# Kernel tuning notes

Measured on AMD Instinct MI355X. Metric: run time of the kernel, lower is better.

Reference implementation:

```python
import jax, jax.numpy as jnp
import numpy as np

N_HEADS = 16
N_UNITS = 1024
B, S = 4, 1024


def setup_inputs() -> dict:
    key = jax.random.key(0)
    ks = jax.random.split(key, 12)
    std = 0.02
    query = jax.random.normal(ks[0], (B, S, N_UNITS), dtype=jnp.float32)
    key_t = jax.random.normal(ks[1], (B, S, N_UNITS), dtype=jnp.float32)
    value = jax.random.normal(ks[2], (B, S, N_UNITS), dtype=jnp.float32)
    # causal mask [B, S, S]; forward does mask.unsqueeze(1) -> broadcast over heads
    mask = jnp.broadcast_to(jnp.tril(jnp.ones((S, S), dtype=jnp.int32)), (B, S, S))
    Wq = jax.random.normal(ks[3], (N_UNITS, N_UNITS), dtype=jnp.float32) * std
    bq = jnp.zeros((N_UNITS,), dtype=jnp.float32)
    Wk = jax.random.normal(ks[4], (N_UNITS, N_UNITS), dtype=jnp.float32) * std
    bk = jnp.zeros((N_UNITS,), dtype=jnp.float32)
    Wv = jax.random.normal(ks[5], (N_UNITS, N_UNITS), dtype=jnp.float32) * std
    bv = jnp.zeros((N_UNITS,), dtype=jnp.float32)
    Wo = jax.random.normal(ks[6], (N_UNITS, N_UNITS), dtype=jnp.float32) * std
    bo = jnp.zeros((N_UNITS,), dtype=jnp.float32)
    return {"query": query, "key": key_t, "value": value, "mask": mask,
            "Wq": Wq, "bq": bq, "Wk": Wk, "bk": bk, "Wv": Wv, "bv": bv,
            "Wo": Wo, "bo": bo}


def reference(query, key, value, mask, Wq, bq, Wk, bk, Wv, bv, Wo, bo):
    b, s, u = query.shape
    h = N_HEADS
    dk = u // h
    # projections (torch Linear: x @ W.T + b), split into heads -> [b, h, s, dk]
    q = (query @ Wq.T + bq).reshape(b, s, h, dk).transpose(0, 2, 1, 3)
    k = (key @ Wk.T + bk).reshape(b, s, h, dk).transpose(0, 2, 1, 3)
    v = (value @ Wv.T + bv).reshape(b, s, h, dk).transpose(0, 2, 1, 3)
    # NOTE: original divides by sqrt(d_k) twice -> net scale 1/d_k (faithful)
    scores = jnp.einsum('bhqd,bhkd->bhqk', q, k) / jnp.float32(dk)
    scores = jnp.where(mask[:, None, :, :] == 0, jnp.float32(-1e9), scores)
    attn = jax.nn.softmax(scores, axis=-1)  # dropout = identity (eval mode)
    out = jnp.einsum('bhqk,bhkd->bhqd', attn, v)
    out = out.transpose(0, 2, 1, 3).reshape(b, s, u)
    return out @ Wo.T + bo
```

## Files before the change

### kernel.cpp

```cpp
#include <hip/hip_runtime.h>
#include <stdint.h>

#define NH 16
#define DK 64
#define NB 4
#define SS 1024
#define UU 1024

typedef __attribute__((ext_vector_type(8))) __bf16 bf16x8;
typedef __attribute__((ext_vector_type(4))) float f32x4;

__device__ inline short f2bf(float f) {
  union { float f; uint32_t u; } c; c.f = f;
  uint32_t u = c.u;
  uint32_t r = (u + 0x7fffu + ((u >> 16) & 1u)) >> 16;
  return (short)(uint16_t)r;
}

__global__ void cvt_multi(const float* __restrict__ s0, const float* __restrict__ s1,
                          const float* __restrict__ s2, const float* __restrict__ s3,
                          short* __restrict__ dst, int n4each) {
  const int z = blockIdx.z;
  const float* s = (z == 0) ? s0 : (z == 1) ? s1 : (z == 2) ? s2 : s3;
  int i = blockIdx.x * blockDim.x + threadIdx.x;
  if (i >= n4each) return;
  const float4 v = reinterpret_cast<const float4*>(s)[i];
  short4 o;
  o.x = f2bf(v.x); o.y = f2bf(v.y); o.z = f2bf(v.z); o.w = f2bf(v.w);
  reinterpret_cast<short4*>(dst + (size_t)z * n4each * 4)[i] = o;
}

template <int ROWS>
__device__ inline void stage_rows(short* lds, const short* gsrc, int ld) {
  const int t = threadIdx.x;
  const int w = t >> 6;
  constexpr int ROUNDS = ROWS / 64;
#pragma unroll
  for (int r = 0; r < ROUNDS; ++r) {
    int idx = r * 256 + t;
    const short* src = gsrc + (size_t)(idx >> 2) * ld + (idx & 3) * 8;
    __builtin_amdgcn_global_load_lds(
        (const __attribute__((address_space(1))) void*)src,
        (__attribute__((address_space(3))) void*)(lds + (size_t)(r * 256 + (w << 6)) * 8),
        16, 0, 0);
  }
}

#define BK 32
#define QSCALE 0.015625f


#define STAGEQ(BI)                                                            \
  {                                                                           \
    stage_rows<128>(AsAll + ((BI) % 3) * (128 * BK), Abf + (size_t)m0 * UU + (BI) * BK, UU); \
    stage_rows<128>(BsAll + ((BI) % 3) * (128 * BK), Bt + (BI) * BK, UU);     \
  }

#define BODYQ(BI, VMC, ...)                                                   \
  {                                                                           \
    asm volatile("s_waitcnt vmcnt(" VMC ")" ::: "memory");                    \
    __builtin_amdgcn_sched_barrier(0);                                        \
    __builtin_amdgcn_s_barrier();                                             \
    __builtin_amdgcn_sched_barrier(0);                                        \
    __VA_ARGS__                                                               \
    __builtin_amdgcn_sched_barrier(0);                                        \
    {                                                                         \
      const short* AsC_ = AsAll + ((BI) % 3) * (128 * BK);                    \
      const short* BsC_ = BsAll + ((BI) % 3) * (128 * BK);                    \
      bf16x8 af[4], bfr[4];                                                   \
      _Pragma("unroll") for (int i = 0; i < 4; ++i)                           \
          af[i] = *(const bf16x8*)&AsC_[(wr * 64 + i * 16 + lr) * BK + lg * 8]; \
      _Pragma("unroll") for (int j = 0; j < 4; ++j)                           \
          bfr[j] = *(const bf16x8*)&BsC_[(wc * 64 + j * 16 + lr) * BK + lg * 8]; \
      _Pragma("unroll") for (int i = 0; i < 4; ++i)                           \
          _Pragma("unroll") for (int j = 0; j < 4; ++j)                       \
              acc[i][j] = __builtin_amdgcn_mfma_f32_16x16x32_bf16(af[i], bfr[j], acc[i][j], 0, 0, 0); \
    }                                                                         \
  }

__global__ void gemm_qkv(const short* __restrict__ xq, const short* __restrict__ xk,
                         const short* __restrict__ xv, const short* __restrict__ wq,
                         const short* __restrict__ wk, const short* __restrict__ wv,
                         const float* __restrict__ bq, const float* __restrict__ bk,
                         const float* __restrict__ bv, short* __restrict__ qb,
                         short* __restrict__ kb, short* __restrict__ vT) {
  __shared__ short AsAll[3 * 128 * BK];
  __shared__ short BsAll[3 * 128 * BK];
  const int bid = blockIdx.x;
  const int g = bid & 7, s2 = bid >> 3;
  const int P = g + (s2 >> 3) * 8;
  const int xt = s2 & 7;
  const int which = P >> 5;
  const int m0 = (P & 31) * 128;
  const int n0 = xt * 128;

  const short* Abf = (which == 0) ? xq : (which == 1) ? xk : xv;
  const short* Bt = ((which == 0) ? wq : (which == 1) ? wk : wv) + (size_t)n0 * UU;
  const float* bias = (which == 0) ? bq : (which == 1) ? bk : bv;

  const int t = threadIdx.x;
  const int w = t >> 6, l = t & 63, lg = l >> 4, lr = l & 15;
  const int wr = w >> 1, wc = w & 1;

  f32x4 acc[4][4];
#pragma unroll
  for (int i = 0; i < 4; ++i)
#pragma unroll
    for (int j = 0; j < 4; ++j) acc[i][j] = (f32x4){0.f, 0.f, 0.f, 0.f};

  STAGEQ(0);
  STAGEQ(1);
  for (int bi = 0; bi < 30; ++bi) {
    BODYQ(bi, "4", STAGEQ(bi + 2);)
  }
  BODYQ(30, "4", ;)
  BODYQ(31, "0", ;)

#pragma unroll
  for (int i = 0; i < 4; ++i) {
#pragma unroll
    for (int j = 0; j < 4; ++j) {
      const int col = n0 + wc * 64 + j * 16 + lr;
      const float bv2 = bias[col];
#pragma unroll
      for (int r = 0; r < 4; ++r) {
        const int row = m0 + wr * 64 + i * 16 + lg * 4 + r;
        float v = acc[i][j][r] + bv2;
        if (which == 0) v *= QSCALE;
        const int b = row >> 10, s = row & 1023;
        const int h = col >> 6, d = col & 63;
        if (which < 2) {
          short* outp = (which == 0) ? qb : kb;
          outp[((size_t)(b * NH + h) * SS + s) * DK + d] = f2bf(v);
        } else {
          vT[((size_t)(b * NH + h) * DK + d) * SS + s] = f2bf(v);
        }
      }
    }
  }
}

#define STAGEO(BI)                                                            \
  {                                                                           \
    stage_rows<128>(AsAll + ((BI) % 3) * (128 * BK), A + (size_t)m0 * K + (BI) * BK, K); \
    stage_rows<64>(BsAll3 + ((BI) % 3) * (64 * BK), Bt + (size_t)n0 * K + (BI) * BK, K); \
  }

#define BODYO(BI, VMC, ...)                                                   \
  {                                                                           \
    asm volatile("s_waitcnt vmcnt(" VMC ")" ::: "memory");                    \
    __builtin_amdgcn_sched_barrier(0);                                        \
    __builtin_amdgcn_s_barrier();                                             \
    __builtin_amdgcn_sched_barrier(0);                                        \
    __VA_ARGS__                                                               \
    __builtin_amdgcn_sched_barrier(0);                                        \
    {                                                                         \
      const short* AsC_ = AsAll + ((BI) % 3) * (128 * BK);                    \
      const short* BsC_ = BsAll3 + ((BI) % 3) * (64 * BK);                    \
      bf16x8 af[4], bfr[2];                                                   \
      _Pragma("unroll") for (int i = 0; i < 4; ++i)                           \
          af[i] = *(const bf16x8*)&AsC_[(wr * 64 + i * 16 + lr) * BK + lg * 8]; \
      _Pragma("unroll") for (int j = 0; j < 2; ++j)                           \
          bfr[j] = *(const bf16x8*)&BsC_[(wc * 32 + j * 16 + lr) * BK + lg * 8]; \
      _Pragma("unroll") for (int i = 0; i < 4; ++i)                           \
          _Pragma("unroll") for (int j = 0; j < 2; ++j)                       \
              acc[i][j] = __builtin_amdgcn_mfma_f32_16x16x32_bf16(af[i], bfr[j], acc[i][j], 0, 0, 0); \
    }                                                                         \
  }

__global__ void gemm_out(const short* __restrict__ A, const short* __restrict__ Bt,
                         const float* __restrict__ bias, float* __restrict__ out,
                         int M, int N, int K) {
  __shared__ short AsAll[3 * 128 * BK];
  __shared__ short BsAll3[3 * 64 * BK];
  const int bid = blockIdx.x;
  const int g = bid & 7, s2 = bid >> 3;
  const int y = g + (s2 >> 4) * 8;
  const int xt = s2 & 15;
  const int m0 = y * 128, n0 = xt * 64;

  const int t = threadIdx.x;
  const int w = t >> 6, l = t & 63, lg = l >> 4, lr = l & 15;
  const int wr = w >> 1, wc = w & 1;

  f32x4 acc[4][2];
#pragma unroll
  for (int i = 0; i < 4; ++i)
#pragma unroll
    for (int j = 0; j < 2; ++j) acc[i][j] = (f32x4){0.f, 0.f, 0.f, 0.f};

  STAGEO(0);
  STAGEO(1);
  for (int bi = 0; bi < 30; ++bi) {
    BODYO(bi, "3", STAGEO(bi + 2);)
  }
  BODYO(30, "3", ;)
  BODYO(31, "0", ;)

#pragma unroll
  for (int i = 0; i < 4; ++i) {
#pragma unroll
    for (int j = 0; j < 2; ++j) {
      const int col = n0 + wc * 32 + j * 16 + lr;
      const float bv = bias[col];
#pragma unroll
      for (int r = 0; r < 4; ++r) {
        const int row = m0 + wr * 64 + i * 16 + lg * 4 + r;
        out[(size_t)row * N + col] = acc[i][j][r] + bv;
      }
    }
  }
}

__global__ void attn_fused(const short* __restrict__ Qh, const short* __restrict__ Kh,
                           const short* __restrict__ VT, short* __restrict__ Ctx) {
  __shared__ short Ks[2][4096];
  __shared__ short Vs[2][4096];
  __shared__ short Pl[4][1024];

  const int bid = blockIdx.x;
  const int g = bid & 7, s2 = bid >> 3;
  const int bh = g + (s2 >> 3) * 8;
  const int xp = s2 & 7;

  const int t = threadIdx.x;
  const int w = t >> 6, l = t & 63, lg = l >> 4, lr = l & 15;
  const short* Qp = Qh + (size_t)bh * SS * DK;
  const short* Kp = Kh + (size_t)bh * SS * DK;
  const short* Vp = VT + (size_t)bh * DK * SS;
  short* Pw = Pl[w];
  const int b = bh >> 4, h = bh & 15;
  const int rowloc = w * 16 + lg * 4;

  int lofs[2], gofK[2], gofV[2];
#pragma unroll
  for (int r = 0; r < 2; ++r) {
    const int idx = r * 256 + t;
    const int L = idx << 4;
    const int Lp = L ^ (((L >> 7) & 7) << 4);
    lofs[r] = (r * 256 + (w << 6)) * 8;
    gofK[r] = (Lp >> 7) * DK + ((Lp & 127) >> 1);
    gofV[r] = (Lp >> 7) * SS + ((Lp & 127) >> 1);
  }

  for (int half = 0; half < 2; ++half) {
    const int qt = half ? (15 - xp) : xp;
    const int q0 = qt * 64 + w * 16;
    const int nt = qt + 1;

    bf16x8 qf[2];
#pragma unroll
    for (int c = 0; c < 2; ++c)
      qf[c] = *(const bf16x8*)&Qp[(q0 + lr) * DK + c * 32 + lg * 8];

    f32x4 o[4];
    float lsum[4];
#pragma unroll
    for (int i = 0; i < 4; ++i) { o[i] = (f32x4){0.f, 0.f, 0.f, 0.f}; lsum[i] = 0.f; }

#pragma unroll
    for (int r = 0; r < 2; ++r)
      __builtin_amdgcn_global_load_lds(
          (const __attribute__((address_space(1))) void*)(Kp + gofK[r]),
          (__attribute__((address_space(3))) void*)(Ks[0] + lofs[r]), 16, 0, 0);
#pragma unroll
    for (int r = 0; r < 2; ++r)
      __builtin_amdgcn_global_load_lds(
          (const __attribute__((address_space(1))) void*)(Vp + gofV[r]),
          (__attribute__((address_space(3))) void*)(Vs[0] + lofs[r]), 16, 0, 0);

    for (int tt = 0; tt < nt; ++tt) {
      const int cb = tt & 1, nb = cb ^ 1;
      if (tt + 1 < nt) {
        const size_t koff = (size_t)(tt + 1) * 64;
#pragma unroll
        for (int r = 0; r < 2; ++r)
          __builtin_amdgcn_global_load_lds(
              (const __attribute__((address_space(1))) void*)(Kp + koff * DK + gofK[r]),
              (__attribute__((address_space(3))) void*)(Ks[nb] + lofs[r]), 16, 0, 0);
#pragma unroll
        for (int r = 0; r < 2; ++r)
          __builtin_amdgcn_global_load_lds(
              (const __attribute__((address_space(1))) void*)(Vp + koff + gofV[r]),
              (__attribute__((address_space(3))) void*)(Vs[nb] + lofs[r]), 16, 0, 0);
        asm volatile("s_waitcnt vmcnt(4)" ::: "memory");
      } else {
        asm volatile("s_waitcnt vmcnt(0)" ::: "memory");
      }
      __builtin_amdgcn_sched_barrier(0);
      __builtin_amdgcn_s_barrier();
      __builtin_amdgcn_sched_barrier(0);

      const short* Kt = Ks[cb];
      const short* Vt = Vs[cb];

      f32x4 sacc[4];
#pragma unroll
      for (int nf = 0; nf < 4; ++nf) sacc[nf] = (f32x4){0.f, 0.f, 0.f, 0.f};
#pragma unroll
      for (int nf = 0; nf < 4; ++nf)
#pragma unroll
        for (int c = 0; c < 2; ++c) {
          const int row = nf * 16 + lr;
          const int Lb = (row << 7) + c * 64 + lg * 16;
          bf16x8 kf = *(const bf16x8*)((const char*)Kt + (Lb ^ ((row & 7) << 4)));
          sacc[nf] = __builtin_amdgcn_mfma_f32_16x16x32_bf16(qf[c], kf, sacc[nf], 0, 0, 0);
        }

      const bool diag = (tt == qt);
#pragma unroll
      for (int nf = 0; nf < 4; ++nf) {
        const int colloc = nf * 16 + lr;
#pragma unroll
        for (int r = 0; r < 4; ++r) {
          float s = sacc[nf][r];
          if (diag && colloc > (rowloc + r)) s = -1.0e9f;
          float p = __expf(s);
          lsum[r] += p;
          const int prow = lg * 4 + r;
          const int boff = (prow * 128 + colloc * 2) ^ ((prow & 7) << 4);
          Pw[boff >> 1] = f2bf(p);
        }
      }

      asm volatile("s_waitcnt lgkmcnt(0)" ::: "memory");
      __builtin_amdgcn_sched_barrier(0);

      bf16x8 pf[2];
#pragma unroll
      for (int c2 = 0; c2 < 2; ++c2) {
        const int boff = (lr * 128 + (c2 * 32 + lg * 8) * 2) ^ ((lr & 7) << 4);
        pf[c2] = *(const bf16x8*)((const char*)Pw + boff);
      }
#pragma unroll
      for (int df = 0; df < 4; ++df)
#pragma unroll
        for (int c2 = 0; c2 < 2; ++c2) {
          const int row = df * 16 + lr;
          const int Lb = (row << 7) + c2 * 64 + lg * 16;
          bf16x8 vf = *(const bf16x8*)((const char*)Vt + (Lb ^ ((row & 7) << 4)));
          o[df] = __builtin_amdgcn_mfma_f32_16x16x32_bf16(pf[c2], vf, o[df], 0, 0, 0);
        }
      __builtin_amdgcn_sched_barrier(0);
      __builtin_amdgcn_s_barrier();
    }

#pragma unroll
    for (int r = 0; r < 4; ++r) {
#pragma unroll
      for (int d = 1; d < 16; d <<= 1)
        lsum[r] += __shfl_xor(lsum[r], d, 64);
    }
    float inv[4];
#pragma unroll
    for (int r = 0; r < 4; ++r) inv[r] = 1.0f / lsum[r];
#pragma unroll
    for (int df = 0; df < 4; ++df)
#pragma unroll
      for (int r = 0; r < 4; ++r) {
        const int qg = q0 + lg * 4 + r;
        Ctx[((size_t)(b * SS + qg)) * UU + h * DK + df * 16 + lr] = f2bf(o[df][r] * inv[r]);
      }
  }
}

extern "C" void kernel_launch(void* const* d_in, const int* in_sizes, int n_in,
                              void* d_out, int out_size, void* d_ws, size_t ws_size,
                              hipStream_t stream) {
  const float* query = (const float*)d_in[0];
  const float* key   = (const float*)d_in[1];
  const float* value = (const float*)d_in[2];
  const float* Wq = (const float*)d_in[4];
  const float* bq = (const float*)d_in[5];
  const float* Wk = (const float*)d_in[6];
  const float* bk = (const float*)d_in[7];
  const float* Wv = (const float*)d_in[8];
  const float* bv = (const float*)d_in[9];
  const float* Wo = (const float*)d_in[10];
  const float* bo = (const float*)d_in[11];
  float* out = (float*)d_out;

  char* ws = (char*)d_ws;
  const size_t MT = (size_t)NB * SS;
  short* qb  = (short*)ws;
  short* kb  = qb + MT * UU;
  short* vT  = kb + MT * UU;
  short* ctx = vT + MT * UU;
  short* xq  = ctx + MT * UU;
  short* xk  = xq + MT * UU;
  short* xv  = xk + MT * UU;
  short* wq  = xv + MT * UU;
  short* wk  = wq + (size_t)UU * UU;
  short* wv  = wk + (size_t)UU * UU;
  short* wo  = wv + (size_t)UU * UU;

  const int TPB = 256;
  {
    int n4 = (int)(MT * UU / 4);
    hipLaunchKernelGGL(cvt_multi, dim3(n4 / TPB, 1, 3), dim3(TPB), 0, stream,
                       query, key, value, query, xq, n4);
  }
  {
    int n4 = (int)((size_t)UU * UU / 4);
    hipLaunchKernelGGL(cvt_multi, dim3(n4 / TPB, 1, 4), dim3(TPB), 0, stream,
                       Wq, Wk, Wv, Wo, wq, n4);
  }

  hipLaunchKernelGGL(gemm_qkv, dim3(768), dim3(TPB), 0, stream,
                     xq, xk, xv, wq, wk, wv, bq, bk, bv, qb, kb, vT);

  hipLaunchKernelGGL(attn_fused, dim3(512), dim3(TPB), 0, stream, qb, kb, vT, ctx);

  hipLaunchKernelGGL(gemm_out, dim3(512), dim3(TPB), 0, stream,
                     ctx, wo, bo, out, (int)MT, UU, UU);
}
```

Measured before the change: 214.8 us.

## Merge conversion launches, widen out-proj tiles, triple-buffer attention K/V, add setprio

```diff
diff --git a/kernel.cpp b/kernel.cpp
--- a/kernel.cpp
+++ b/kernel.cpp
@@ -17,17 +17,27 @@
   return (short)(uint16_t)r;
 }
 
-__global__ void cvt_multi(const float* __restrict__ s0, const float* __restrict__ s1,
-                          const float* __restrict__ s2, const float* __restrict__ s3,
-                          short* __restrict__ dst, int n4each) {
-  const int z = blockIdx.z;
-  const float* s = (z == 0) ? s0 : (z == 1) ? s1 : (z == 2) ? s2 : s3;
-  int i = blockIdx.x * blockDim.x + threadIdx.x;
-  if (i >= n4each) return;
-  const float4 v = reinterpret_cast<const float4*>(s)[i];
+__global__ void cvt_all(const float* __restrict__ q, const float* __restrict__ k,
+                        const float* __restrict__ v, const float* __restrict__ wq,
+                        const float* __restrict__ wk, const float* __restrict__ wv,
+                        const float* __restrict__ wo, short* __restrict__ dst) {
+  const int i = blockIdx.x * blockDim.x + threadIdx.x;
+  const float* s;
+  int local;
+  if (i < 3 * 1048576) {
+    const int z = i >> 20;
+    local = i & 1048575;
+    s = (z == 0) ? q : (z == 1) ? k : v;
+  } else {
+    const int j = i - 3 * 1048576;
+    const int z = j >> 18;
+    local = j & 262143;
+    s = (z == 0) ? wq : (z == 1) ? wk : (z == 2) ? wv : wo;
+  }
+  const float4 vv = reinterpret_cast<const float4*>(s)[local];
   short4 o;
-  o.x = f2bf(v.x); o.y = f2bf(v.y); o.z = f2bf(v.z); o.w = f2bf(v.w);
-  reinterpret_cast<short4*>(dst + (size_t)z * n4each * 4)[i] = o;
+  o.x = f2bf(vv.x); o.y = f2bf(vv.y); o.z = f2bf(vv.z); o.w = f2bf(vv.w);
+  reinterpret_cast<short4*>(dst)[i] = o;
 }
 
 template <int ROWS>
@@ -48,7 +58,6 @@
 
 #define BK 32
 #define QSCALE 0.015625f
-
 
 #define STAGEQ(BI)                                                            \
   {                                                                           \
@@ -140,13 +149,13 @@
   }
 }
 
-#define STAGEO(BI)                                                            \
+#define STAGEW(BI)                                                            \
   {                                                                           \
-    stage_rows<128>(AsAll + ((BI) % 3) * (128 * BK), A + (size_t)m0 * K + (BI) * BK, K); \
-    stage_rows<64>(BsAll3 + ((BI) % 3) * (64 * BK), Bt + (size_t)n0 * K + (BI) * BK, K); \
-  }
-
-#define BODYO(BI, VMC, ...)                                                   \
+    stage_rows<128>(AsAll + ((BI) % 3) * (128 * BK), A + (size_t)m0 * UU + (BI) * BK, UU); \
+    stage_rows<128>(BsAll + ((BI) % 3) * (128 * BK), Bt + (size_t)n0 * UU + (BI) * BK, UU); \
+  }
+
+#define BODYW(BI, VMC, ...)                                                   \
   {                                                                           \
     asm volatile("s_waitcnt vmcnt(" VMC ")" ::: "memory");                    \
     __builtin_amdgcn_sched_barrier(0);                                        \
@@ -156,57 +165,56 @@
     __builtin_amdgcn_sched_barrier(0);                                        \
     {                                                                         \
       const short* AsC_ = AsAll + ((BI) % 3) * (128 * BK);                    \
-      const short* BsC_ = BsAll3 + ((BI) % 3) * (64 * BK);                    \
-      bf16x8 af[4], bfr[2];                                                   \
+      const short* BsC_ = BsAll + ((BI) % 3) * (128 * BK);                    \
+      bf16x8 af[4], bfr[4];                                                   \
       _Pragma("unroll") for (int i = 0; i < 4; ++i)                           \
           af[i] = *(const bf16x8*)&AsC_[(wr * 64 + i * 16 + lr) * BK + lg * 8]; \
-      _Pragma("unroll") for (int j = 0; j < 2; ++j)                           \
-          bfr[j] = *(const bf16x8*)&BsC_[(wc * 32 + j * 16 + lr) * BK + lg * 8]; \
+      _Pragma("unroll") for (int j = 0; j < 4; ++j)                           \
+          bfr[j] = *(const bf16x8*)&BsC_[(wc * 64 + j * 16 + lr) * BK + lg * 8]; \
       _Pragma("unroll") for (int i = 0; i < 4; ++i)                           \
-          _Pragma("unroll") for (int j = 0; j < 2; ++j)                       \
+          _Pragma("unroll") for (int j = 0; j < 4; ++j)                       \
               acc[i][j] = __builtin_amdgcn_mfma_f32_16x16x32_bf16(af[i], bfr[j], acc[i][j], 0, 0, 0); \
     }                                                                         \
   }
 
 __global__ void gemm_out(const short* __restrict__ A, const short* __restrict__ Bt,
-                         const float* __restrict__ bias, float* __restrict__ out,
-                         int M, int N, int K) {
+                         const float* __restrict__ bias, float* __restrict__ out) {
   __shared__ short AsAll[3 * 128 * BK];
-  __shared__ short BsAll3[3 * 64 * BK];
+  __shared__ short BsAll[3 * 128 * BK];
   const int bid = blockIdx.x;
   const int g = bid & 7, s2 = bid >> 3;
-  const int y = g + (s2 >> 4) * 8;
-  const int xt = s2 & 15;
-  const int m0 = y * 128, n0 = xt * 64;
+  const int y = g + (s2 >> 3) * 8;
+  const int xt = s2 & 7;
+  const int m0 = y * 128, n0 = xt * 128;
 
   const int t = threadIdx.x;
   const int w = t >> 6, l = t & 63, lg = l >> 4, lr = l & 15;
   const int wr = w >> 1, wc = w & 1;
 
-  f32x4 acc[4][2];
+  f32x4 acc[4][4];
 #pragma unroll
   for (int i = 0; i < 4; ++i)
 #pragma unroll
-    for (int j = 0; j < 2; ++j) acc[i][j] = (f32x4){0.f, 0.f, 0.f, 0.f};
-
-  STAGEO(0);
-  STAGEO(1);
+    for (int j = 0; j < 4; ++j) acc[i][j] = (f32x4){0.f, 0.f, 0.f, 0.f};
+
+  STAGEW(0);
+  STAGEW(1);
   for (int bi = 0; bi < 30; ++bi) {
-    BODYO(bi, "3", STAGEO(bi + 2);)
-  }
-  BODYO(30, "3", ;)
-  BODYO(31, "0", ;)
+    BODYW(bi, "4", STAGEW(bi + 2);)
+  }
+  BODYW(30, "4", ;)
+  BODYW(31, "0", ;)
 
 #pragma unroll
   for (int i = 0; i < 4; ++i) {
 #pragma unroll
-    for (int j = 0; j < 2; ++j) {
-      const int col = n0 + wc * 32 + j * 16 + lr;
+    for (int j = 0; j < 4; ++j) {
+      const int col = n0 + wc * 64 + j * 16 + lr;
       const float bv = bias[col];
 #pragma unroll
       for (int r = 0; r < 4; ++r) {
         const int row = m0 + wr * 64 + i * 16 + lg * 4 + r;
-        out[(size_t)row * N + col] = acc[i][j][r] + bv;
+        out[(size_t)row * UU + col] = acc[i][j][r] + bv;
       }
     }
   }
@@ -214,8 +222,8 @@
 
 __global__ void attn_fused(const short* __restrict__ Qh, const short* __restrict__ Kh,
                            const short* __restrict__ VT, short* __restrict__ Ctx) {
-  __shared__ short Ks[2][4096];
-  __shared__ short Vs[2][4096];
+  __shared__ short Ks[3][4096];
+  __shared__ short Vs[3][4096];
   __shared__ short Pl[4][1024];
 
   const int bid = blockIdx.x;
@@ -243,6 +251,19 @@
     gofV[r] = (Lp >> 7) * SS + ((Lp & 127) >> 1);
   }
 
+#define STAGEKV(TI, BUF)                                                      \
+  {                                                                           \
+    const size_t koff_ = (size_t)(TI) * 64;                                   \
+    _Pragma("unroll") for (int r = 0; r < 2; ++r)                             \
+        __builtin_amdgcn_global_load_lds(                                     \
+            (const __attribute__((address_space(1))) void*)(Kp + koff_ * DK + gofK[r]), \
+            (__attribute__((address_space(3))) void*)(Ks[BUF] + lofs[r]), 16, 0, 0); \
+    _Pragma("unroll") for (int r = 0; r < 2; ++r)                             \
+        __builtin_amdgcn_global_load_lds(                                     \
+            (const __attribute__((address_space(1))) void*)(Vp + koff_ + gofV[r]), \
+            (__attribute__((address_space(3))) void*)(Vs[BUF] + lofs[r]), 16, 0, 0); \
+  }
+
   for (int half = 0; half < 2; ++half) {
     const int qt = half ? (15 - xp) : xp;
     const int q0 = qt * 64 + w * 16;
@@ -258,31 +279,15 @@
 #pragma unroll
     for (int i = 0; i < 4; ++i) { o[i] = (f32x4){0.f, 0.f, 0.f, 0.f}; lsum[i] = 0.f; }
 
-#pragma unroll
-    for (int r = 0; r < 2; ++r)
-      __builtin_amdgcn_global_load_lds(
-          (const __attribute__((address_space(1))) void*)(Kp + gofK[r]),
-          (__attribute__((address_space(3))) void*)(Ks[0] + lofs[r]), 16, 0, 0);
-#pragma unroll
-    for (int r = 0; r < 2; ++r)
-      __builtin_amdgcn_global_load_lds(
-          (const __attribute__((address_space(1))) void*)(Vp + gofV[r]),
-          (__attribute__((address_space(3))) void*)(Vs[0] + lofs[r]), 16, 0, 0);
+    STAGEKV(0, 0);
+    if (nt > 1) STAGEKV(1, 1);
 
     for (int tt = 0; tt < nt; ++tt) {
-      const int cb = tt & 1, nb = cb ^ 1;
-      if (tt + 1 < nt) {
-        const size_t koff = (size_t)(tt + 1) * 64;
-#pragma unroll
-        for (int r = 0; r < 2; ++r)
-          __builtin_amdgcn_global_load_lds(
-              (const __attribute__((address_space(1))) void*)(Kp + koff * DK + gofK[r]),
-              (__attribute__((address_space(3))) void*)(Ks[nb] + lofs[r]), 16, 0, 0);
-#pragma unroll
-        for (int r = 0; r < 2; ++r)
-          __builtin_amdgcn_global_load_lds(
-              (const __attribute__((address_space(1))) void*)(Vp + koff + gofV[r]),
-              (__attribute__((address_space(3))) void*)(Vs[nb] + lofs[r]), 16, 0, 0);
+      const int cb = tt % 3;
+      if (tt + 2 < nt) {
+        STAGEKV(tt + 2, (tt + 2) % 3);
+        asm volatile("s_waitcnt vmcnt(8)" ::: "memory");
+      } else if (tt + 1 < nt) {
         asm volatile("s_waitcnt vmcnt(4)" ::: "memory");
       } else {
         asm volatile("s_waitcnt vmcnt(0)" ::: "memory");
@@ -293,10 +298,12 @@
 
       const short* Kt = Ks[cb];
       const short* Vt = Vs[cb];
+      const int kk0 = tt * 64;
 
       f32x4 sacc[4];
 #pragma unroll
       for (int nf = 0; nf < 4; ++nf) sacc[nf] = (f32x4){0.f, 0.f, 0.f, 0.f};
+      __builtin_amdgcn_s_setprio(1);
 #pragma unroll
       for (int nf = 0; nf < 4; ++nf)
 #pragma unroll
@@ -306,6 +313,7 @@
           bf16x8 kf = *(const bf16x8*)((const char*)Kt + (Lb ^ ((row & 7) << 4)));
           sacc[nf] = __builtin_amdgcn_mfma_f32_16x16x32_bf16(qf[c], kf, sacc[nf], 0, 0, 0);
         }
+      __builtin_amdgcn_s_setprio(0);
 
       const bool diag = (tt == qt);
 #pragma unroll
@@ -332,6 +340,7 @@
         const int boff = (lr * 128 + (c2 * 32 + lg * 8) * 2) ^ ((lr & 7) << 4);
         pf[c2] = *(const bf16x8*)((const char*)Pw + boff);
       }
+      __builtin_amdgcn_s_setprio(1);
 #pragma unroll
       for (int df = 0; df < 4; ++df)
 #pragma unroll
@@ -341,6 +350,7 @@
           bf16x8 vf = *(const bf16x8*)((const char*)Vt + (Lb ^ ((row & 7) << 4)));
           o[df] = __builtin_amdgcn_mfma_f32_16x16x32_bf16(pf[c2], vf, o[df], 0, 0, 0);
         }
+      __builtin_amdgcn_s_setprio(0);
       __builtin_amdgcn_sched_barrier(0);
       __builtin_amdgcn_s_barrier();
     }
@@ -362,6 +372,7 @@
         Ctx[((size_t)(b * SS + qg)) * UU + h * DK + df * 16 + lr] = f2bf(o[df][r] * inv[r]);
       }
   }
+#undef STAGEKV
 }
 
 extern "C" void kernel_launch(void* const* d_in, const int* in_sizes, int n_in,
@@ -395,22 +406,13 @@
   short* wo  = wv + (size_t)UU * UU;
 
   const int TPB = 256;
-  {
-    int n4 = (int)(MT * UU / 4);
-    hipLaunchKernelGGL(cvt_multi, dim3(n4 / TPB, 1, 3), dim3(TPB), 0, stream,
-                       query, key, value, query, xq, n4);
-  }
-  {
-    int n4 = (int)((size_t)UU * UU / 4);
-    hipLaunchKernelGGL(cvt_multi, dim3(n4 / TPB, 1, 4), dim3(TPB), 0, stream,
-                       Wq, Wk, Wv, Wo, wq, n4);
-  }
+  hipLaunchKernelGGL(cvt_all, dim3(4194304 / TPB), dim3(TPB), 0, stream,
+                     query, key, value, Wq, Wk, Wv, Wo, xq);
 
   hipLaunchKernelGGL(gemm_qkv, dim3(768), dim3(TPB), 0, stream,
                      xq, xk, xv, wq, wk, wv, bq, bk, bv, qb, kb, vT);
 
   hipLaunchKernelGGL(attn_fused, dim3(512), dim3(TPB), 0, stream, qb, kb, vT, ctx);
 
-  hipLaunchKernelGGL(gemm_out, dim3(512), dim3(TPB), 0, stream,
-                     ctx, wo, bo, out, (int)MT, UU, UU);
-}
+  hipLaunchKernelGGL(gemm_out, dim3(256), dim3(TPB), 0, stream, ctx, wo, bo, out);
+}
```

Result: no change. 218.3 us (+1.6%).
